# Kernel optimization log

Hardware: AMD Instinct MI355X
Metric: run time of the kernel (lower is better)

## Reference

```python
import jax, jax.numpy as jnp
import numpy as np

HIDDEN = 1024
NUM_HEADS = 16
HEAD = HIDDEN // NUM_HEADS
B, S = 2, 2048


def setup_inputs() -> dict:
    key = jax.random.key(0)
    ks = jax.random.split(key, 7)
    scale = 1.0 / np.sqrt(HIDDEN)
    return {
        "hidden_states": jax.random.normal(ks[0], (B, S, HIDDEN), dtype=jnp.float32),
        "Wq": jax.random.normal(ks[1], (HIDDEN, HIDDEN), dtype=jnp.float32) * scale,
        "bq": jax.random.normal(ks[2], (HIDDEN,), dtype=jnp.float32) * 0.01,
        "Wk": jax.random.normal(ks[3], (HIDDEN, HIDDEN), dtype=jnp.float32) * scale,
        "bk": jax.random.normal(ks[4], (HIDDEN,), dtype=jnp.float32) * 0.01,
        "Wv": jax.random.normal(ks[5], (HIDDEN, HIDDEN), dtype=jnp.float32) * scale,
        "bv": jax.random.normal(ks[6], (HIDDEN,), dtype=jnp.float32) * 0.01,
    }


def _split_heads(x):
    b, s, _ = x.shape
    return x.reshape(b, s, NUM_HEADS, HEAD).transpose(0, 2, 1, 3)  # [B,H,S,D]


def reference(hidden_states, Wq, bq, Wk, bk, Wv, bv):
    # Linear projections (dropout is inference no-op)
    Q = _split_heads(hidden_states @ Wq + bq)
    K = _split_heads(hidden_states @ Wk + bk)
    V = _split_heads(hidden_states @ Wv + bv)
    scores = jnp.einsum("bhqd,bhkd->bhqk", Q, K) / np.sqrt(HEAD).astype(np.float32)
    probs = jax.nn.softmax(scores, axis=-1)
    context = jnp.einsum("bhqk,bhkd->bhqd", probs, V)  # [B,H,S,D]
    return context.transpose(0, 2, 1, 3).reshape(B, S, HIDDEN)
```

## Files before the change

### kernel.cpp

```cpp
#include <hip/hip_runtime.h>
#include <hip/hip_bf16.h>

typedef __bf16 bf16_t;
typedef __bf16 bf16x4v __attribute__((ext_vector_type(4)));
typedef __bf16 bf16x8 __attribute__((ext_vector_type(8)));
typedef float f32x4 __attribute__((ext_vector_type(4)));
typedef float f32x16 __attribute__((ext_vector_type(16)));
typedef unsigned short u16;
typedef unsigned int u32;
typedef u16 u16x8 __attribute__((ext_vector_type(8)));

#define HIDDEN 1024
#define NHEAD 16
#define HEADD 64
#define BATCH 2
#define SEQ 2048
#define TOKENS (BATCH*SEQ)

#define Z16 {0.f,0.f,0.f,0.f,0.f,0.f,0.f,0.f,0.f,0.f,0.f,0.f,0.f,0.f,0.f,0.f}
#define M12F -12.0f
#define M16 {M12F,M12F,M12F,M12F,M12F,M12F,M12F,M12F,M12F,M12F,M12F,M12F,M12F,M12F,M12F,M12F}

__global__ __launch_bounds__(256) void k_transpose_w(const float* __restrict__ Wq,
                                                     const float* __restrict__ Wk,
                                                     const float* __restrict__ Wv,
                                                     bf16_t* __restrict__ wt) {
  int mat = blockIdx.z;
  const float* W = (mat == 0) ? Wq : (mat == 1 ? Wk : Wv);
  bf16_t* dst = wt + (size_t)mat * HIDDEN * HIDDEN;
  __shared__ float tile[32][33];
  int k0 = blockIdx.x * 32, n0 = blockIdx.y * 32;
  int tc = threadIdx.x & 31, tr = threadIdx.x >> 5;
#pragma unroll
  for (int r = 0; r < 32; r += 8)
    tile[tr + r][tc] = W[(size_t)(k0 + tr + r) * HIDDEN + n0 + tc];
  __syncthreads();
#pragma unroll
  for (int r = 0; r < 32; r += 8)
    dst[(size_t)(n0 + tr + r) * HIDDEN + k0 + tc] = (bf16_t)tile[tc][tr + r];
}

__global__ __launch_bounds__(512, 3) void k_gemm_qkv(
    const float* __restrict__ hs, const bf16_t* __restrict__ wt,
    const float* __restrict__ bq, const float* __restrict__ bk,
    const float* __restrict__ bv, bf16_t* __restrict__ Qo,
    bf16_t* __restrict__ Ko, bf16_t* __restrict__ Vo) {
  __shared__ bf16x8 As[2][4 * 128];
  __shared__ bf16x8 Bs[2][4 * 256];
  int t = threadIdx.x;
  int wave = t >> 6, lane = t & 63;
  int m0 = blockIdx.x * 128;
  int nb = blockIdx.y;
  int mat = nb >> 2;
  int n0 = (nb & 3) * 256;
  const bf16_t* Wmat = wt + (size_t)mat * HIDDEN * HIDDEN;
  const float* bias = (mat == 0) ? bq : (mat == 1 ? bk : bv);
  bf16_t* dst = (mat == 0) ? Qo : (mat == 1 ? Ko : Vo);

  int wm = wave >> 2, wn = wave & 3;
  int lrow = lane & 15;
  int lc = lane >> 4;

  f32x4 acc[4][4];
#pragma unroll
  for (int a = 0; a < 4; ++a)
#pragma unroll
    for (int b = 0; b < 4; ++b) acc[a][b] = (f32x4){0.f, 0.f, 0.f, 0.f};

  bf16x8 ra, rb[2];
  auto load_tiles = [&](int kt) {
    int k0 = kt * 32;
    {
      int row = t >> 2, c = t & 3;
      const float* ap = hs + (size_t)(m0 + row) * HIDDEN + k0 + c * 8;
      float4 f0 = *(const float4*)(ap);
      float4 f1 = *(const float4*)(ap + 4);
      bf16x8 v;
      v[0] = (bf16_t)f0.x; v[1] = (bf16_t)f0.y; v[2] = (bf16_t)f0.z; v[3] = (bf16_t)f0.w;
      v[4] = (bf16_t)f1.x; v[5] = (bf16_t)f1.y; v[6] = (bf16_t)f1.z; v[7] = (bf16_t)f1.w;
      ra = v;
    }
#pragma unroll
    for (int u = 0; u < 2; ++u) {
      int id = t + u * 512;
      int row = id >> 2, c = id & 3;
      rb[u] = *(const bf16x8*)(Wmat + (size_t)(n0 + row) * HIDDEN + k0 + c * 8);
    }
  };
  auto store_tiles = [&](int buf) {
    {
      int row = t >> 2, c = t & 3;
      As[buf][c * 128 + (row ^ c)] = ra;
    }
#pragma unroll
    for (int u = 0; u < 2; ++u) {
      int id = t + u * 512;
      int row = id >> 2, c = id & 3;
      Bs[buf][c * 256 + (row ^ c)] = rb[u];
    }
  };

  load_tiles(0);
  store_tiles(0);
  __syncthreads();
  const int NT = HIDDEN / 32;
  int cur = 0;
  for (int kt = 0; kt < NT; ++kt) {
    if (kt + 1 < NT) load_tiles(kt + 1);
    bf16x8 af[4], bfr[4];
#pragma unroll
    for (int fm = 0; fm < 4; ++fm)
      af[fm] = As[cur][lc * 128 + ((wm * 64 + fm * 16 + lrow) ^ lc)];
#pragma unroll
    for (int fn = 0; fn < 4; ++fn)
      bfr[fn] = Bs[cur][lc * 256 + ((wn * 64 + fn * 16 + lrow) ^ lc)];
#pragma unroll
    for (int fm = 0; fm < 4; ++fm)
#pragma unroll
      for (int fn = 0; fn < 4; ++fn)
        acc[fm][fn] = __builtin_amdgcn_mfma_f32_16x16x32_bf16(
            af[fm], bfr[fn], acc[fm][fn], 0, 0, 0);
    if (kt + 1 < NT) store_tiles(cur ^ 1);
    __syncthreads();
    cur ^= 1;
  }

  float scale = (mat == 0) ? 0.18033688011112042f : 1.0f;
#pragma unroll
  for (int fm = 0; fm < 4; ++fm) {
#pragma unroll
    for (int fn = 0; fn < 4; ++fn) {
      int n = n0 + wn * 64 + fn * 16 + (lane & 15);
      float bval = bias[n];
      int h = n >> 6, d = n & 63;
      int mbase = m0 + wm * 64 + fm * 16 + (lane >> 4) * 4;
      int b = mbase >> 11, s = mbase & 2047;
      if (mat == 2) {
        bf16x4v pk;
#pragma unroll
        for (int j = 0; j < 4; ++j) pk[j] = (bf16_t)(acc[fm][fn][j] + bval);
        *(bf16x4v*)(dst + ((size_t)(b * NHEAD + h) * HEADD + d) * SEQ + s) = pk;
      } else {
#pragma unroll
        for (int j = 0; j < 4; ++j) {
          float v = (acc[fm][fn][j] + bval) * scale;
          dst[((size_t)(b * NHEAD + h) * SEQ + (s + j)) * HEADD + d] = (bf16_t)v;
        }
      }
    }
  }
}

__device__ __forceinline__ void gload16(const void* g, void* l) {
  __builtin_amdgcn_global_load_lds((const __attribute__((address_space(1))) u32*)g,
                                   (__attribute__((address_space(3))) u32*)l, 16, 0, 0);
}

__global__ __launch_bounds__(512, 4) void k_attn(const bf16_t* __restrict__ Q,
                                                 const bf16_t* __restrict__ K,
                                                 const bf16_t* __restrict__ Vt,
                                                 float* __restrict__ out) {
  __shared__ __align__(16) char smem[66560];
  const int t = threadIdx.x;
  const int w = t >> 6, l = t & 63;
  const int g = w >> 2, wg = w & 3;
  const int hi = l >> 5;
  const int l31 = l & 31;
  const int lx = l & 7;

  const int n_hw = blockIdx.x + 16 * blockIdx.y;
  const int work = (n_hw & 7) * 64 + (n_hw >> 3);
  const int qt = work & 15;
  const int bh = work >> 4;
  const int b = bh >> 4, h = bh & 15;
  const char* Kp = (const char*)(K + (size_t)bh * SEQ * HEADD) + (size_t)g * 1024 * 128;
  const char* Vp = (const char*)(Vt + (size_t)bh * HEADD * SEQ) + (size_t)g * 1024 * 2;
  const bf16_t* Qp = Q + (size_t)bh * SEQ * HEADD;

  const int q0 = qt * 128 + wg * 32;

  bf16x8 qa[4];
#pragma unroll
  for (int ds = 0; ds < 4; ++ds)
    qa[ds] = *(const bf16x8*)(Qp + (size_t)(q0 + l31) * HEADD + ds * 16 + hi * 8);

  f32x16 o0 = (f32x16)(0.f), o1 = (f32x16)(0.f);
  float l_run = 0.f;

  char* gK = smem + g * 32768;
  char* gV = gK + 16384;
  const int srow = wg * 16 + (l >> 3);
  const int sg = lx ^ (l >> 3);

  auto stage = [&](int tile, int buf) {
#pragma unroll
    for (int s = 0; s < 2; ++s) {
      int row = srow + 8 * s;
      gload16(Kp + (size_t)(tile * 64 + row) * 128 + sg * 16,
              gK + buf * 8192 + wg * 2048 + s * 1024);
      gload16(Vp + (size_t)row * (SEQ * 2) + tile * 128 + sg * 16,
              gV + buf * 8192 + wg * 2048 + s * 1024);
    }
  };

  stage(0, 0);
  __syncthreads();

  int roff0[4], roff1[4];
#pragma unroll
  for (int ds = 0; ds < 4; ++ds) {
    roff0[ds] = l31 * 128 + ((2 * ds + hi) ^ lx) * 16;
    roff1[ds] = (32 + l31) * 128 + ((2 * ds + hi) ^ lx) * 16;
  }

  const f32x16 minit = M16;
  int cur = 0;
  for (int r = 0; r < 16; ++r) {
    if (r < 15) stage(r + 1, cur ^ 1);
    const char* Kc = gK + cur * 8192;
    const char* Vc = gV + cur * 8192;

    f32x16 s0 = minit, s1 = minit;
    __builtin_amdgcn_s_setprio(1);
#pragma unroll
    for (int ds = 0; ds < 4; ++ds) {
      bf16x8 kf0 = *(const bf16x8*)(Kc + roff0[ds]);
      s0 = __builtin_amdgcn_mfma_f32_32x32x16_bf16(kf0, qa[ds], s0, 0, 0, 0);
      bf16x8 kf1 = *(const bf16x8*)(Kc + roff1[ds]);
      s1 = __builtin_amdgcn_mfma_f32_32x32x16_bf16(kf1, qa[ds], s1, 0, 0, 0);
    }
    __builtin_amdgcn_s_setprio(0);

#pragma unroll
    for (int i = 0; i < 16; ++i) {
      s0[i] = __builtin_amdgcn_exp2f(s0[i]);
      s1[i] = __builtin_amdgcn_exp2f(s1[i]);
    }
    {
      float ta[16];
#pragma unroll
      for (int i = 0; i < 16; ++i) ta[i] = s0[i] + s1[i];
#pragma unroll
      for (int i = 0; i < 8; ++i) ta[i] += ta[i + 8];
#pragma unroll
      for (int i = 0; i < 4; ++i) ta[i] += ta[i + 4];
      l_run += (ta[0] + ta[1]) + (ta[2] + ta[3]);
    }

    bf16x8 pf[4];
    {
      u32 u[16];
#pragma unroll
      for (int i = 0; i < 8; ++i) {
        union { bf16_t h[2]; u32 ww; } c0, c1;
        c0.h[0] = (bf16_t)s0[2 * i]; c0.h[1] = (bf16_t)s0[2 * i + 1];
        c1.h[0] = (bf16_t)s1[2 * i]; c1.h[1] = (bf16_t)s1[2 * i + 1];
        u[i] = c0.ww; u[8 + i] = c1.ww;
      }
#pragma unroll
      for (int gg = 0; gg < 4; ++gg) {
        u32 a0 = u[4 * gg + 0], b0 = u[4 * gg + 2];
        u32 a1 = u[4 * gg + 1], b1 = u[4 * gg + 3];
        asm("v_permlane32_swap_b32 %0, %1" : "+v"(a0), "+v"(b0));
        asm("v_permlane32_swap_b32 %0, %1" : "+v"(a1), "+v"(b1));
        union { u32 wv[4]; bf16x8 v; } fu;
        fu.wv[0] = a0; fu.wv[1] = a1; fu.wv[2] = b0; fu.wv[3] = b1;
        pf[gg] = fu.v;
      }
    }

    __builtin_amdgcn_s_setprio(1);
#pragma unroll
    for (int kblk = 0; kblk < 4; ++kblk) {
      bf16x8 vf0 = *(const bf16x8*)(Vc + roff0[kblk]);
      o0 = __builtin_amdgcn_mfma_f32_32x32x16_bf16(vf0, pf[kblk], o0, 0, 0, 0);
      bf16x8 vf1 = *(const bf16x8*)(Vc + roff1[kblk]);
      o1 = __builtin_amdgcn_mfma_f32_32x32x16_bf16(vf1, pf[kblk], o1, 0, 0, 0);
    }
    __builtin_amdgcn_s_setprio(0);
    __syncthreads();
    cur ^= 1;
  }

  float l_half = l_run + __shfl_xor(l_run, 32);
  float* OL = (float*)(smem + g * 32768);
  const int orow = wg * 32 + l31;
#pragma unroll
  for (int j = 0; j < 16; ++j) {
    int dv0 = (j & 3) + 8 * (j >> 2) + 4 * hi;
    OL[orow * 64 + ((dv0 + orow) & 63)] = o0[j];
    int dv1 = 32 + dv0;
    OL[orow * 64 + ((dv1 + orow) & 63)] = o1[j];
  }
  float* LL = (float*)(smem + 65536);
  if (hi == 0) LL[g * 128 + orow] = l_half;
  __syncthreads();
  {
    int ql = t >> 2;
    int dvb = (t & 3) * 16;
    float inv = 1.0f / (LL[ql] + LL[128 + ql]);
    const float* A = (const float*)smem;
    const float* B = (const float*)(smem + 32768);
    float* op = out + ((size_t)b * SEQ + qt * 128 + ql) * HIDDEN + h * HEADD + dvb;
#pragma unroll
    for (int g4 = 0; g4 < 4; ++g4) {
      f32x4 v4;
#pragma unroll
      for (int e = 0; e < 4; ++e) {
        int dv = dvb + g4 * 4 + e;
        int idx = ql * 64 + ((dv + ql) & 63);
        v4[e] = (A[idx] + B[idx]) * inv;
      }
      *(f32x4*)(op + g4 * 4) = v4;
    }
  }
}

extern "C" void kernel_launch(void* const* d_in, const int* in_sizes, int n_in,
                              void* d_out, int out_size, void* d_ws, size_t ws_size,
                              hipStream_t stream) {
  const float* hs = (const float*)d_in[0];
  const float* Wq = (const float*)d_in[1];
  const float* bq = (const float*)d_in[2];
  const float* Wk = (const float*)d_in[3];
  const float* bk = (const float*)d_in[4];
  const float* Wv = (const float*)d_in[5];
  const float* bv = (const float*)d_in[6];
  float* out = (float*)d_out;
  char* ws = (char*)d_ws;

  const size_t SZ_X = (size_t)TOKENS * HIDDEN * 2;
  const size_t SZ_W = (size_t)3 * HIDDEN * HIDDEN * 2;
  const size_t SZ_P = (size_t)TOKENS * HIDDEN * 2;
  bf16_t* Wt = (bf16_t*)(ws + SZ_X);
  bf16_t* Qb = (bf16_t*)(ws + SZ_X + SZ_W);
  bf16_t* Kb = (bf16_t*)(ws + SZ_X + SZ_W + SZ_P);
  bf16_t* Vb = (bf16_t*)(ws + SZ_X + SZ_W + 2 * SZ_P);

  k_transpose_w<<<dim3(32, 32, 3), 256, 0, stream>>>(Wq, Wk, Wv, Wt);
  k_gemm_qkv<<<dim3(32, 12), 512, 0, stream>>>(hs, Wt, bq, bk, bv, Qb, Kb, Vb);
  k_attn<<<dim3(16, 32), 512, 0, stream>>>(Qb, Kb, Vb, out);
}
```

Baseline: 101.8 us.

## Have each attention wave process 64 queries, halving waves per block

```diff
diff --git a/kernel.cpp b/kernel.cpp
--- a/kernel.cpp
+++ b/kernel.cpp
@@ -17,7 +17,6 @@
 #define SEQ 2048
 #define TOKENS (BATCH*SEQ)
 
-#define Z16 {0.f,0.f,0.f,0.f,0.f,0.f,0.f,0.f,0.f,0.f,0.f,0.f,0.f,0.f,0.f,0.f}
 #define M12F -12.0f
 #define M16 {M12F,M12F,M12F,M12F,M12F,M12F,M12F,M12F,M12F,M12F,M12F,M12F,M12F,M12F,M12F,M12F}
 
@@ -156,14 +155,48 @@
                                    (__attribute__((address_space(3))) u32*)l, 16, 0, 0);
 }
 
-__global__ __launch_bounds__(512, 4) void k_attn(const bf16_t* __restrict__ Q,
+#define TREESUM(sA, sB, L)                                                   \
+  do {                                                                       \
+    float ta[16];                                                            \
+    _Pragma("unroll")                                                        \
+    for (int i = 0; i < 16; ++i) ta[i] = sA[i] + sB[i];                      \
+    _Pragma("unroll")                                                        \
+    for (int i = 0; i < 8; ++i) ta[i] += ta[i + 8];                          \
+    _Pragma("unroll")                                                        \
+    for (int i = 0; i < 4; ++i) ta[i] += ta[i + 4];                          \
+    L += (ta[0] + ta[1]) + (ta[2] + ta[3]);                                  \
+  } while (0)
+
+#define PACK(sA, sB, PF)                                                     \
+  do {                                                                       \
+    u32 u[16];                                                               \
+    _Pragma("unroll")                                                        \
+    for (int i = 0; i < 8; ++i) {                                            \
+      union { bf16_t hh[2]; u32 ww; } c0, c1;                                \
+      c0.hh[0] = (bf16_t)sA[2 * i]; c0.hh[1] = (bf16_t)sA[2 * i + 1];        \
+      c1.hh[0] = (bf16_t)sB[2 * i]; c1.hh[1] = (bf16_t)sB[2 * i + 1];        \
+      u[i] = c0.ww; u[8 + i] = c1.ww;                                        \
+    }                                                                        \
+    _Pragma("unroll")                                                        \
+    for (int gg = 0; gg < 4; ++gg) {                                         \
+      u32 a0 = u[4 * gg + 0], b0 = u[4 * gg + 2];                            \
+      u32 a1 = u[4 * gg + 1], b1 = u[4 * gg + 3];                            \
+      asm("v_permlane32_swap_b32 %0, %1" : "+v"(a0), "+v"(b0));              \
+      asm("v_permlane32_swap_b32 %0, %1" : "+v"(a1), "+v"(b1));              \
+      union { u32 wv[4]; bf16x8 v; } fu;                                     \
+      fu.wv[0] = a0; fu.wv[1] = a1; fu.wv[2] = b0; fu.wv[3] = b1;            \
+      PF[gg] = fu.v;                                                         \
+    }                                                                        \
+  } while (0)
+
+__global__ __launch_bounds__(256, 2) void k_attn(const bf16_t* __restrict__ Q,
                                                  const bf16_t* __restrict__ K,
                                                  const bf16_t* __restrict__ Vt,
                                                  float* __restrict__ out) {
   __shared__ __align__(16) char smem[66560];
   const int t = threadIdx.x;
   const int w = t >> 6, l = t & 63;
-  const int g = w >> 2, wg = w & 3;
+  const int g = w >> 1, qh = w & 1;
   const int hi = l >> 5;
   const int l31 = l & 31;
   const int lx = l & 7;
@@ -177,29 +210,32 @@
   const char* Vp = (const char*)(Vt + (size_t)bh * HEADD * SEQ) + (size_t)g * 1024 * 2;
   const bf16_t* Qp = Q + (size_t)bh * SEQ * HEADD;
 
-  const int q0 = qt * 128 + wg * 32;
-
-  bf16x8 qa[4];
-#pragma unroll
-  for (int ds = 0; ds < 4; ++ds)
-    qa[ds] = *(const bf16x8*)(Qp + (size_t)(q0 + l31) * HEADD + ds * 16 + hi * 8);
-
-  f32x16 o0 = (f32x16)(0.f), o1 = (f32x16)(0.f);
-  float l_run = 0.f;
+  const int q0w = qt * 128 + qh * 64;
+
+  bf16x8 qa0[4], qa1[4];
+#pragma unroll
+  for (int ds = 0; ds < 4; ++ds) {
+    qa0[ds] = *(const bf16x8*)(Qp + (size_t)(q0w + l31) * HEADD + ds * 16 + hi * 8);
+    qa1[ds] = *(const bf16x8*)(Qp + (size_t)(q0w + 32 + l31) * HEADD + ds * 16 + hi * 8);
+  }
+
+  f32x16 o00 = (f32x16)(0.f), o01 = (f32x16)(0.f);
+  f32x16 o10 = (f32x16)(0.f), o11 = (f32x16)(0.f);
+  float l_run0 = 0.f, l_run1 = 0.f;
 
   char* gK = smem + g * 32768;
   char* gV = gK + 16384;
-  const int srow = wg * 16 + (l >> 3);
+  const int srow = qh * 32 + (l >> 3);
   const int sg = lx ^ (l >> 3);
 
   auto stage = [&](int tile, int buf) {
 #pragma unroll
-    for (int s = 0; s < 2; ++s) {
+    for (int s = 0; s < 4; ++s) {
       int row = srow + 8 * s;
       gload16(Kp + (size_t)(tile * 64 + row) * 128 + sg * 16,
-              gK + buf * 8192 + wg * 2048 + s * 1024);
+              gK + buf * 8192 + qh * 4096 + s * 1024);
       gload16(Vp + (size_t)row * (SEQ * 2) + tile * 128 + sg * 16,
-              gV + buf * 8192 + wg * 2048 + s * 1024);
+              gV + buf * 8192 + qh * 4096 + s * 1024);
     }
   };
 
@@ -220,14 +256,16 @@
     const char* Kc = gK + cur * 8192;
     const char* Vc = gV + cur * 8192;
 
-    f32x16 s0 = minit, s1 = minit;
+    f32x16 s0 = minit, s1 = minit, s2 = minit, s3 = minit;
     __builtin_amdgcn_s_setprio(1);
 #pragma unroll
     for (int ds = 0; ds < 4; ++ds) {
       bf16x8 kf0 = *(const bf16x8*)(Kc + roff0[ds]);
-      s0 = __builtin_amdgcn_mfma_f32_32x32x16_bf16(kf0, qa[ds], s0, 0, 0, 0);
       bf16x8 kf1 = *(const bf16x8*)(Kc + roff1[ds]);
-      s1 = __builtin_amdgcn_mfma_f32_32x32x16_bf16(kf1, qa[ds], s1, 0, 0, 0);
+      s0 = __builtin_amdgcn_mfma_f32_32x32x16_bf16(kf0, qa0[ds], s0, 0, 0, 0);
+      s1 = __builtin_amdgcn_mfma_f32_32x32x16_bf16(kf1, qa0[ds], s1, 0, 0, 0);
+      s2 = __builtin_amdgcn_mfma_f32_32x32x16_bf16(kf0, qa1[ds], s2, 0, 0, 0);
+      s3 = __builtin_amdgcn_mfma_f32_32x32x16_bf16(kf1, qa1[ds], s3, 0, 0, 0);
     }
     __builtin_amdgcn_s_setprio(0);
 
@@ -235,75 +273,59 @@
     for (int i = 0; i < 16; ++i) {
       s0[i] = __builtin_amdgcn_exp2f(s0[i]);
       s1[i] = __builtin_amdgcn_exp2f(s1[i]);
-    }
-    {
-      float ta[16];
-#pragma unroll
-      for (int i = 0; i < 16; ++i) ta[i] = s0[i] + s1[i];
-#pragma unroll
-      for (int i = 0; i < 8; ++i) ta[i] += ta[i + 8];
-#pragma unroll
-      for (int i = 0; i < 4; ++i) ta[i] += ta[i + 4];
-      l_run += (ta[0] + ta[1]) + (ta[2] + ta[3]);
-    }
-
-    bf16x8 pf[4];
-    {
-      u32 u[16];
-#pragma unroll
-      for (int i = 0; i < 8; ++i) {
-        union { bf16_t h[2]; u32 ww; } c0, c1;
-        c0.h[0] = (bf16_t)s0[2 * i]; c0.h[1] = (bf16_t)s0[2 * i + 1];
-        c1.h[0] = (bf16_t)s1[2 * i]; c1.h[1] = (bf16_t)s1[2 * i + 1];
-        u[i] = c0.ww; u[8 + i] = c1.ww;
-      }
-#pragma unroll
-      for (int gg = 0; gg < 4; ++gg) {
-        u32 a0 = u[4 * gg + 0], b0 = u[4 * gg + 2];
-        u32 a1 = u[4 * gg + 1], b1 = u[4 * gg + 3];
-        asm("v_permlane32_swap_b32 %0, %1" : "+v"(a0), "+v"(b0));
-        asm("v_permlane32_swap_b32 %0, %1" : "+v"(a1), "+v"(b1));
-        union { u32 wv[4]; bf16x8 v; } fu;
-        fu.wv[0] = a0; fu.wv[1] = a1; fu.wv[2] = b0; fu.wv[3] = b1;
-        pf[gg] = fu.v;
-      }
-    }
+      s2[i] = __builtin_amdgcn_exp2f(s2[i]);
+      s3[i] = __builtin_amdgcn_exp2f(s3[i]);
+    }
+    TREESUM(s0, s1, l_run0);
+    TREESUM(s2, s3, l_run1);
+
+    bf16x8 pf0[4], pf1[4];
+    PACK(s0, s1, pf0);
+    PACK(s2, s3, pf1);
 
     __builtin_amdgcn_s_setprio(1);
 #pragma unroll
     for (int kblk = 0; kblk < 4; ++kblk) {
       bf16x8 vf0 = *(const bf16x8*)(Vc + roff0[kblk]);
-      o0 = __builtin_amdgcn_mfma_f32_32x32x16_bf16(vf0, pf[kblk], o0, 0, 0, 0);
       bf16x8 vf1 = *(const bf16x8*)(Vc + roff1[kblk]);
-      o1 = __builtin_amdgcn_mfma_f32_32x32x16_bf16(vf1, pf[kblk], o1, 0, 0, 0);
+      o00 = __builtin_amdgcn_mfma_f32_32x32x16_bf16(vf0, pf0[kblk], o00, 0, 0, 0);
+      o01 = __builtin_amdgcn_mfma_f32_32x32x16_bf16(vf1, pf0[kblk], o01, 0, 0, 0);
+      o10 = __builtin_amdgcn_mfma_f32_32x32x16_bf16(vf0, pf1[kblk], o10, 0, 0, 0);
+      o11 = __builtin_amdgcn_mfma_f32_32x32x16_bf16(vf1, pf1[kblk], o11, 0, 0, 0);
     }
     __builtin_amdgcn_s_setprio(0);
     __syncthreads();
     cur ^= 1;
   }
 
-  float l_half = l_run + __shfl_xor(l_run, 32);
+  float l_h0 = l_run0 + __shfl_xor(l_run0, 32);
+  float l_h1 = l_run1 + __shfl_xor(l_run1, 32);
   float* OL = (float*)(smem + g * 32768);
-  const int orow = wg * 32 + l31;
+  const int orow0 = qh * 64 + l31;
+  const int orow1 = qh * 64 + 32 + l31;
 #pragma unroll
   for (int j = 0; j < 16; ++j) {
     int dv0 = (j & 3) + 8 * (j >> 2) + 4 * hi;
-    OL[orow * 64 + ((dv0 + orow) & 63)] = o0[j];
-    int dv1 = 32 + dv0;
-    OL[orow * 64 + ((dv1 + orow) & 63)] = o1[j];
+    OL[orow0 * 64 + ((dv0 + orow0) & 63)] = o00[j];
+    OL[orow0 * 64 + ((dv0 + 32 + orow0) & 63)] = o01[j];
+    OL[orow1 * 64 + ((dv0 + orow1) & 63)] = o10[j];
+    OL[orow1 * 64 + ((dv0 + 32 + orow1) & 63)] = o11[j];
   }
   float* LL = (float*)(smem + 65536);
-  if (hi == 0) LL[g * 128 + orow] = l_half;
+  if (hi == 0) {
+    LL[g * 128 + orow0] = l_h0;
+    LL[g * 128 + orow1] = l_h1;
+  }
   __syncthreads();
   {
-    int ql = t >> 2;
-    int dvb = (t & 3) * 16;
+    int ql = t >> 1;
+    int dvb = (t & 1) * 32;
     float inv = 1.0f / (LL[ql] + LL[128 + ql]);
     const float* A = (const float*)smem;
     const float* B = (const float*)(smem + 32768);
     float* op = out + ((size_t)b * SEQ + qt * 128 + ql) * HIDDEN + h * HEADD + dvb;
 #pragma unroll
-    for (int g4 = 0; g4 < 4; ++g4) {
+    for (int g4 = 0; g4 < 8; ++g4) {
       f32x4 v4;
 #pragma unroll
       for (int e = 0; e < 4; ++e) {
@@ -339,5 +361,5 @@
 
   k_transpose_w<<<dim3(32, 32, 3), 256, 0, stream>>>(Wq, Wk, Wv, Wt);
   k_gemm_qkv<<<dim3(32, 12), 512, 0, stream>>>(hs, Wt, bq, bk, bv, Qb, Kb, Vb);
-  k_attn<<<dim3(16, 32), 512, 0, stream>>>(Qb, Kb, Vb, out);
-}
+  k_attn<<<dim3(16, 32), 256, 0, stream>>>(Qb, Kb, Vb, out);
+}
```

New measurement: 96.62 us, median of 3. -5.1%, faster.
